# Performance work log

Measured on AMD Instinct MI355X. Metric: run time of the kernel, lower is better.

## Reference

```python
import jax, jax.numpy as jnp
import numpy as np

B, S, D = 4, 2048, 1024
H = 16
HD = D // H


def setup_inputs() -> dict:
    key = jax.random.key(0)
    ks = jax.random.split(key, 6)
    s = 1.0 / np.sqrt(D)
    x = jax.random.normal(ks[0], (B, S, D), dtype=jnp.float32)
    Wq = jax.random.uniform(ks[1], (D, D), jnp.float32, -s, s)
    Wk = jax.random.uniform(ks[2], (D, D), jnp.float32, -s, s)
    Wv = jax.random.uniform(ks[3], (D, D), jnp.float32, -s, s)
    Wo = jax.random.uniform(ks[4], (D, D), jnp.float32, -s, s)
    bo = jax.random.uniform(ks[5], (D,), jnp.float32, -s, s)
    return {"x": x, "Wq": Wq, "Wk": Wk, "Wv": Wv, "Wo": Wo, "bo": bo}


def reference(x, Wq, Wk, Wv, Wo, bo):
    b, n, _ = x.shape
    # QKV projections (nn.Linear applies x @ W.T; W here stored as [d_in, d_out])
    q = (x @ Wq).reshape(b, n, H, HD).transpose(0, 2, 1, 3)  # [b,h,s,hd]
    k = (x @ Wk).reshape(b, n, H, HD).transpose(0, 2, 1, 3)
    v = (x @ Wv).reshape(b, n, H, HD).transpose(0, 2, 1, 3)
    scores = jnp.einsum('bhqd,bhkd->bhqk', q, k) / np.sqrt(HD).astype(np.float32)
    causal = jnp.tril(jnp.ones((n, n), dtype=bool))  # True = keep
    scores = jnp.where(causal, scores, -jnp.inf)
    attn = jax.nn.softmax(scores, axis=-1)
    ctx = jnp.einsum('bhqk,bhkd->bhqd', attn, v)  # [b,h,s,hd]
    ctx = ctx.transpose(0, 2, 1, 3).reshape(b, n, D)
    return ctx @ Wo + bo
```

## Files before the change

kernel.cpp:

```cpp
#include <hip/hip_runtime.h>

#define NB 4
#define NS 2048
#define ND 1024
#define NH 16
#define NHD 64
#define NTOK (NB*NS)

typedef float f32x4 __attribute__((ext_vector_type(4)));
typedef __bf16 bf16x8 __attribute__((ext_vector_type(8)));
typedef __bf16 bf16x4 __attribute__((ext_vector_type(4)));

#define MFMA16(a,b,c) __builtin_amdgcn_mfma_f32_16x16x32_bf16((a),(b),(c),0,0,0)
#define SBAR() __builtin_amdgcn_s_barrier()
#define VMCNT(n) asm volatile("s_waitcnt vmcnt(" #n ")" ::: "memory")
#define LGKM(n) asm volatile("s_waitcnt lgkmcnt(" #n ")" ::: "memory")
#define SCHEDB() __builtin_amdgcn_sched_barrier(0)

__device__ __forceinline__ float fexp2(float x) {
#if __has_builtin(__builtin_amdgcn_exp2f)
  return __builtin_amdgcn_exp2f(x);
#else
  return __expf(x * 0.69314718056f);
#endif
}

__device__ __forceinline__ void gload_lds16(const __bf16* g, const __bf16* l) {
  __builtin_amdgcn_global_load_lds(
      (const __attribute__((address_space(1))) void*)(uintptr_t)(const void*)g,
      (__attribute__((address_space(3))) void*)(uint32_t)(uintptr_t)(const void*)l,
      16, 0, 0);
}

__global__ void k_convert_x(const float* __restrict__ x, __bf16* __restrict__ xb) {
  int i = blockIdx.x * blockDim.x + threadIdx.x;
  float4 v = ((const float4*)x)[i];
  bf16x4 o = { (__bf16)v.x, (__bf16)v.y, (__bf16)v.z, (__bf16)v.w };
  ((bf16x4*)xb)[i] = o;
}

__global__ void k_transpose_w(const float* __restrict__ w0, const float* __restrict__ w1,
                              const float* __restrict__ w2, const float* __restrict__ w3,
                              __bf16* __restrict__ wqkvt, __bf16* __restrict__ wot) {
  __shared__ float tl[64][65];
  const int z = blockIdx.z;
  const float* src = (z==0)?w0:(z==1)?w1:(z==2)?w2:w3;
  __bf16* dst = (z<3) ? (wqkvt + (size_t)z*ND*ND) : wot;
  const int kb = blockIdx.x*64, nb = blockIdx.y*64;
  const int c = threadIdx.x & 63, r0 = threadIdx.x >> 6;
  for (int i=0;i<16;i++) { int r = r0*16+i; tl[r][c] = src[(size_t)(kb+r)*ND + nb + c]; }
  __syncthreads();
  for (int i=0;i<16;i++) { int r = r0*16+i; dst[(size_t)(nb+r)*ND + kb + c] = (__bf16)tl[c][r]; }
}

__global__ __launch_bounds__(512, 4) void k_gemm_qkv(
    const __bf16* __restrict__ A, const __bf16* __restrict__ Bt,
    __bf16* __restrict__ qs, __bf16* __restrict__ ks, __bf16* __restrict__ vt) {
  constexpr int BUFE = (256+128)*32;
  __shared__ __align__(16) __bf16 lds[3*BUFE];
  const int tid = threadIdx.x;
  const int wid = tid>>6, lane = tid&63;
  const int wr = wid>>1, wc = wid&1;
  const int lrow = lane&15, lg = lane>>4;
  const int srow4 = lane>>2;
  const int scol  = ((lane&3) ^ ((lane>>3)&3))*8;

  const int id  = blockIdx.x;
  const int xcd = id & 7;
  const int nl  = id >> 3;
  const int st  = nl >> 5;
  const int u   = nl & 31;
  const int bx  = xcd*4 + (u >> 3);
  const int by  = st*8 + (u & 7);
  const int m0 = bx*256, n0 = by*128;

  auto stage = [&](int t, int bsel) {
    __bf16* buf = lds + bsel*BUFE;
    const int k0 = t*32;
    #pragma unroll
    for (int i=0;i<2;i++) {
      int c = wid + i*8;
      gload_lds16(A + (size_t)(m0 + c*16 + srow4)*ND + k0 + scol, buf + c*512);
    }
    gload_lds16(Bt + (size_t)(n0 + wid*16 + srow4)*ND + k0 + scol, buf + 8192 + wid*512);
  };

  const int slot = (lg ^ ((lrow>>1)&3)) << 4;
  const int abase = (wr*64 + lrow)*64 + slot;
  const int bbase = 16384 + (wc*64 + lrow)*64 + slot;

  f32x4 acc[4][4];
  f32x4 zero = {0.f,0.f,0.f,0.f};
  #pragma unroll
  for (int i=0;i<4;i++) for (int j=0;j<4;j++) acc[i][j] = zero;

  stage(0,0);
  stage(1,1);
  for (int t=0; t<32; ++t) {
    if (t < 30) stage(t+2, (t+2)%3);
    if (t < 30)      { VMCNT(6); }
    else if (t == 30){ VMCNT(3); }
    else             { VMCNT(0); }
    SBAR();
    const char* L = (const char*)(lds + (t%3)*BUFE);
    bf16x8 bfr[4], af[4];
    #pragma unroll
    for (int cb=0;cb<4;cb++) bfr[cb] = *(const bf16x8*)(L + bbase + cb*1024);
    #pragma unroll
    for (int mf=0;mf<2;mf++) af[mf] = *(const bf16x8*)(L + abase + mf*1024);
    SCHEDB();
    #pragma unroll
    for (int mf=2;mf<4;mf++) af[mf] = *(const bf16x8*)(L + abase + mf*1024);
    LGKM(2);
    SCHEDB();
    __builtin_amdgcn_s_setprio(1);
    #pragma unroll
    for (int mf=0;mf<2;mf++)
      #pragma unroll
      for (int cb=0;cb<4;cb++)
        acc[mf][cb] = MFMA16(af[mf], bfr[cb], acc[mf][cb]);
    __builtin_amdgcn_s_setprio(0);
    LGKM(0);
    SCHEDB();
    __builtin_amdgcn_s_setprio(1);
    #pragma unroll
    for (int mf=2;mf<4;mf++)
      #pragma unroll
      for (int cb=0;cb<4;cb++)
        acc[mf][cb] = MFMA16(af[mf], bfr[cb], acc[mf][cb]);
    __builtin_amdgcn_s_setprio(0);
    SBAR();
  }

  const int which = by >> 3;
  const int h = (by&7)*2 + wc;
  __bf16* ws = lds + wid*4096;
  const int tokbase = m0 + wr*64;
  const int b = tokbase >> 11, s0 = tokbase & 2047;

  if (which < 2) {
    __bf16* dst = which ? ks : qs;
    #pragma unroll
    for (int mf=0;mf<4;mf++)
      #pragma unroll
      for (int cb=0;cb<4;cb++)
        #pragma unroll
        for (int r=0;r<4;r++) {
          int row = mf*16 + lg*4 + r;
          int chunk = (cb*2 + (lrow>>3)) ^ (row&7);
          *(__bf16*)((char*)ws + row*128 + chunk*16 + (lrow&7)*2) = (__bf16)acc[mf][cb][r];
        }
    #pragma unroll
    for (int p=0;p<8;p++) {
      int row = p*8 + (lane>>3);
      int chunk = (lane&7) ^ (row&7);
      bf16x8 v = *(const bf16x8*)((char*)ws + row*128 + chunk*16);
      *(bf16x8*)(dst + ((size_t)(b*NH + h)*NS + s0 + row)*NHD + (lane&7)*8) = v;
    }
  } else {
    #pragma unroll
    for (int mf=0;mf<4;mf++)
      #pragma unroll
      for (int cb=0;cb<4;cb++) {
        bf16x4 pk = { (__bf16)acc[mf][cb][0], (__bf16)acc[mf][cb][1],
                      (__bf16)acc[mf][cb][2], (__bf16)acc[mf][cb][3] };
        int ldsrow = cb*16 + lrow;
        int chunk = (mf*2 + (lg>>1)) ^ (ldsrow&7);
        *(bf16x4*)((char*)ws + ldsrow*128 + chunk*16 + (lg&1)*8) = pk;
      }
    #pragma unroll
    for (int p=0;p<8;p++) {
      int hd = p*8 + (lane>>3);
      int chunk = (lane&7) ^ (hd&7);
      bf16x8 v = *(const bf16x8*)((char*)ws + hd*128 + chunk*16);
      *(bf16x8*)(vt + ((size_t)(b*NH + h)*NHD + hd)*NS + s0 + (lane&7)*8) = v;
    }
  }
}

__global__ __launch_bounds__(512, 2) void k_gemm_out(
    const __bf16* __restrict__ A, const __bf16* __restrict__ Bt,
    const float* __restrict__ bo, float* __restrict__ out) {
  constexpr int BUFE = (256+128)*64;
  __shared__ __align__(16) __bf16 lds[3*BUFE];
  const int tid = threadIdx.x;
  const int wid = tid>>6, lane = tid&63;
  const int wr = wid>>1, wc = wid&1;
  const int lrow = lane&15, lg = lane>>4;
  const int srow = lane>>3;
  const int scol = ((lane&7) ^ srow)*8;

  const int id  = blockIdx.x;
  const int xcd = id & 7;
  const int nl  = id >> 3;
  const int bx  = xcd*4 + (nl >> 3);
  const int by  = nl & 7;
  const int m0 = bx*256, n0 = by*128;

  auto stage = [&](int t, int bsel) {
    __bf16* buf = lds + bsel*BUFE;
    const int k0 = t*64;
    #pragma unroll
    for (int i=0;i<4;i++) {
      int c = wid + i*8;
      gload_lds16(A + (size_t)(m0 + c*8 + srow)*ND + k0 + scol, buf + c*512);
    }
    #pragma unroll
    for (int i=0;i<2;i++) {
      int c = wid + i*8;
      gload_lds16(Bt + (size_t)(n0 + c*8 + srow)*ND + k0 + scol, buf + 16384 + c*512);
    }
  };

  int kx[8];
  #pragma unroll
  for (int kk=0;kk<8;kk++) kx[kk] = ((kk ^ (lrow&7)) << 4);
  const int abase = (wr*64 + lrow)*128;
  const int bbase = 32768 + (wc*64 + lrow)*128;

  f32x4 acc[4][4];
  f32x4 zero = {0.f,0.f,0.f,0.f};
  #pragma unroll
  for (int i=0;i<4;i++) for (int j=0;j<4;j++) acc[i][j] = zero;

  stage(0,0);
  stage(1,1);
  for (int t=0; t<16; ++t) {
    if (t < 14) stage(t+2, (t+2)%3);
    if (t < 14)      { VMCNT(12); }
    else if (t == 14){ VMCNT(6);  }
    else             { VMCNT(0);  }
    SBAR();
    const char* L = (const char*)(lds + (t%3)*BUFE);
    bf16x8 bfr[4][2], af[4][2];
    #pragma unroll
    for (int cb=0;cb<4;cb++)
      #pragma unroll
      for (int ksi=0;ksi<2;ksi++)
        bfr[cb][ksi] = *(const bf16x8*)(L + bbase + cb*2048 + kx[ksi*4+lg]);
    #pragma unroll
    for (int mf=0;mf<2;mf++)
      #pragma unroll
      for (int ksi=0;ksi<2;ksi++)
        af[mf][ksi] = *(const bf16x8*)(L + abase + mf*2048 + kx[ksi*4+lg]);
    SCHEDB();
    #pragma unroll
    for (int mf=2;mf<4;mf++)
      #pragma unroll
      for (int ksi=0;ksi<2;ksi++)
        af[mf][ksi] = *(const bf16x8*)(L + abase + mf*2048 + kx[ksi*4+lg]);
    LGKM(4);
    SCHEDB();
    __builtin_amdgcn_s_setprio(1);
    #pragma unroll
    for (int mf=0;mf<2;mf++)
      #pragma unroll
      for (int cb=0;cb<4;cb++)
        #pragma unroll
        for (int ksi=0;ksi<2;ksi++)
          acc[mf][cb] = MFMA16(af[mf][ksi], bfr[cb][ksi], acc[mf][cb]);
    __builtin_amdgcn_s_setprio(0);
    LGKM(0);
    SCHEDB();
    __builtin_amdgcn_s_setprio(1);
    #pragma unroll
    for (int mf=2;mf<4;mf++)
      #pragma unroll
      for (int cb=0;cb<4;cb++)
        #pragma unroll
        for (int ksi=0;ksi<2;ksi++)
          acc[mf][cb] = MFMA16(af[mf][ksi], bfr[cb][ksi], acc[mf][cb]);
    __builtin_amdgcn_s_setprio(0);
    SBAR();
  }

  #pragma unroll
  for (int cb=0;cb<4;cb++) {
    const int n = n0 + wc*64 + cb*16 + lrow;
    const float bias = bo[n];
    #pragma unroll
    for (int mf=0;mf<4;mf++)
      #pragma unroll
      for (int r=0;r<4;r++) {
        const int m = m0 + wr*64 + mf*16 + lg*4 + r;
        out[(size_t)m*ND + n] = acc[mf][cb][r] + bias;
      }
  }
}

__global__ __launch_bounds__(256, 3) void k_attn(
    const __bf16* __restrict__ qs, const __bf16* __restrict__ ks,
    const __bf16* __restrict__ vt, __bf16* __restrict__ ctx) {
  __shared__ __align__(16) __bf16 sK[2][64*64];
  __shared__ __align__(16) __bf16 sV[2][64*64];
  __shared__ __align__(16) __bf16 sP[4][32*72];
  const int tid = threadIdx.x, w = tid >> 6, lane = tid & 63;
  const int lrow = lane & 15, lg = lane >> 4;
  const int bh = blockIdx.x;
  const int bq = 15 - blockIdx.y;
  const int nt = 2*bq + 2;
  const size_t base = (size_t)bh * NS * NHD;
  const __bf16* Kg = ks + base;
  const __bf16* Vg = vt + base;
  __bf16* sPw = sP[w];

  const int q0w = bq*128 + w*32;
  bf16x8 qf[2][2];
  for (int rb=0;rb<2;rb++)
    for (int kk=0;kk<2;kk++) {
      bf16x8 v = *(const bf16x8*)(qs + base + (size_t)(q0w + rb*16 + lrow)*NHD + kk*32 + lg*8);
      bf16x8 o;
      for (int j=0;j<8;j++) o[j] = (__bf16)((float)v[j] * 0.1803368801f);
      qf[rb][kk] = o;
    }

  int koffB[4][2];
  for (int cb=0;cb<4;cb++) {
    int r = cb*16 + lrow;
    for (int kk=0;kk<2;kk++)
      koffB[cb][kk] = r*128 + (((kk*4 + lg) ^ (r & 7)) << 4);
  }
  const int s_r[2]  = { (w + 0)*8 + (lane>>3), (w + 4)*8 + (lane>>3) };
  const int s_u[2]  = { (lane&7) ^ (s_r[0]&7), (lane&7) ^ (s_r[1]&7) };

  f32x4 zero = {0.f,0.f,0.f,0.f};
  f32x4 oacc[2][4];
  float psum[2] = {0.f, 0.f};
  for (int rb=0;rb<2;rb++) for(int cb=0;cb<4;cb++) oacc[rb][cb]=zero;

  for (int i=0;i<2;i++) {
    gload_lds16(Kg + (size_t)s_r[i]*NHD + s_u[i]*8,              sK[0] + (w + i*4)*512);
    gload_lds16(Vg + (size_t)s_r[i]*NS  + s_u[i]*8,              sV[0] + (w + i*4)*512);
  }
  asm volatile("s_waitcnt vmcnt(0)" ::: "memory");
  __syncthreads();

  int buf = 0;
  for (int t = 0; t < nt; ++t) {
    if (t+1 < nt) {
      const __bf16* Kt = Kg + (size_t)(t+1)*64*NHD;
      for (int i=0;i<2;i++) {
        gload_lds16(Kt + (size_t)s_r[i]*NHD + s_u[i]*8,          sK[buf^1] + (w + i*4)*512);
        gload_lds16(Vg + (size_t)s_r[i]*NS + (t+1)*64 + s_u[i]*8, sV[buf^1] + (w + i*4)*512);
      }
    }
    if (!(t == nt-1 && w < 2)) {
      const __bf16* bK = sK[buf];
      const __bf16* bV = sV[buf];
      const bool bdry = (t >= nt-2);
      for (int cb=0;cb<4;cb++) {
        bf16x8 kf0 = *(const bf16x8*)((const char*)bK + koffB[cb][0]);
        bf16x8 kf1 = *(const bf16x8*)((const char*)bK + koffB[cb][1]);
        const int kvb = t*64 + cb*16 + lg*4;
        for (int rb=0;rb<2;rb++) {
          f32x4 s4 = MFMA16(kf0, qf[rb][0], zero);
          s4 = MFMA16(kf1, qf[rb][1], s4);
          const int qg = q0w + rb*16 + lrow;
          float e0 = fexp2(s4[0]), e1 = fexp2(s4[1]);
          float e2 = fexp2(s4[2]), e3 = fexp2(s4[3]);
          if (bdry) {
            if (kvb + 0 > qg) e0 = 0.f;
            if (kvb + 1 > qg) e1 = 0.f;
            if (kvb + 2 > qg) e2 = 0.f;
            if (kvb + 3 > qg) e3 = 0.f;
          }
          psum[rb] += (e0 + e1) + (e2 + e3);
          bf16x4 pk = { (__bf16)e0, (__bf16)e1, (__bf16)e2, (__bf16)e3 };
          *(bf16x4*)(sPw + (rb*16 + lrow)*72 + cb*16 + lg*4) = pk;
        }
      }
      for (int kk=0;kk<2;kk++) {
        bf16x8 pa0 = *(const bf16x8*)(sPw + (lrow)*72      + kk*32 + lg*8);
        bf16x8 pa1 = *(const bf16x8*)(sPw + (16 + lrow)*72 + kk*32 + lg*8);
        for (int cb=0;cb<4;cb++) {
          bf16x8 vb = *(const bf16x8*)((const char*)bV + koffB[cb][kk]);
          oacc[0][cb] = MFMA16(pa0, vb, oacc[0][cb]);
          oacc[1][cb] = MFMA16(pa1, vb, oacc[1][cb]);
        }
      }
    }
    asm volatile("s_waitcnt vmcnt(0)" ::: "memory");
    __syncthreads();
    buf ^= 1;
  }

  float inv[2];
  for (int rb=0;rb<2;rb++) {
    float s = psum[rb];
    s += __shfl_xor(s, 16);
    s += __shfl_xor(s, 32);
    inv[rb] = 1.0f / s;
  }

  __bf16* ws = &sK[0][0] + w*2048;
  const int b = bh >> 4, h = bh & 15;
  for (int rb=0;rb<2;rb++)
    for (int cb=0;cb<4;cb++)
      for (int r=0;r<4;r++) {
        int row = rb*16 + lg*4 + r;
        float nrm = __shfl(inv[rb], lg*4 + r);
        int chunk = (cb*2 + (lrow>>3)) ^ (row&7);
        *(__bf16*)((char*)ws + row*128 + chunk*16 + (lrow&7)*2) =
            (__bf16)(oacc[rb][cb][r] * nrm);
      }
  for (int p=0;p<4;p++) {
    int row = p*8 + (lane>>3);
    int chunk = (lane&7) ^ (row&7);
    bf16x8 v = *(const bf16x8*)((char*)ws + row*128 + chunk*16);
    int q = q0w + row;
    *(bf16x8*)(ctx + ((size_t)(b*NS + q))*ND + h*NHD + (lane&7)*8) = v;
  }
}

extern "C" void kernel_launch(void* const* d_in, const int* in_sizes, int n_in,
                              void* d_out, int out_size, void* d_ws, size_t ws_size,
                              hipStream_t stream) {
  const float* x  = (const float*)d_in[0];
  const float* Wq = (const float*)d_in[1];
  const float* Wk = (const float*)d_in[2];
  const float* Wv = (const float*)d_in[3];
  const float* Wo = (const float*)d_in[4];
  const float* bo = (const float*)d_in[5];
  float* out = (float*)d_out;

  __bf16* xb    = (__bf16*)d_ws;
  __bf16* wqkvt = xb    + (size_t)NTOK*ND;
  __bf16* wot   = wqkvt + (size_t)3*ND*ND;
  __bf16* qsc   = wot   + (size_t)ND*ND;
  __bf16* ksc   = qsc   + (size_t)NTOK*ND;
  __bf16* vtc   = ksc   + (size_t)NTOK*ND;
  __bf16* ctx   = vtc   + (size_t)NTOK*ND;

  k_convert_x<<<NTOK*ND/(4*256), 256, 0, stream>>>(x, xb);
  k_transpose_w<<<dim3(ND/64, ND/64, 4), 256, 0, stream>>>(Wq, Wk, Wv, Wo, wqkvt, wot);
  k_gemm_qkv<<<768, 512, 0, stream>>>(xb, wqkvt, qsc, ksc, vtc);
  k_attn<<<dim3(NB*NH, NS/128), 256, 0, stream>>>(qsc, ksc, vtc, ctx);
  k_gemm_out<<<256, 512, 0, stream>>>(ctx, wot, bo, out);
}
```

Measured before the change: 145.1 us.

## Double QKV GEMM K-tile and interleave prefetch with MFMA quarters; merge prep kernels

The QKV GEMM now stages 64-wide K tiles instead of 32, which halves the number of main-loop iterations. It uses a new 8-way XOR swizzle and splits each iteration into four MFMA quarters, with the next tile's global-to-LDS loads issued between them. This is meant to cut barrier and loop overhead and to hide load latency behind compute. LDS use doubles, so occupancy drops and launch_bounds is lowered to 2 blocks per unit. The x conversion and weight transpose kernels are also merged into a single launch to save one kernel launch.

```diff
diff --git a/kernel.cpp b/kernel.cpp
--- a/kernel.cpp
+++ b/kernel.cpp
@@ -32,38 +32,41 @@
       16, 0, 0);
 }
 
-__global__ void k_convert_x(const float* __restrict__ x, __bf16* __restrict__ xb) {
-  int i = blockIdx.x * blockDim.x + threadIdx.x;
-  float4 v = ((const float4*)x)[i];
-  bf16x4 o = { (__bf16)v.x, (__bf16)v.y, (__bf16)v.z, (__bf16)v.w };
-  ((bf16x4*)xb)[i] = o;
-}
-
-__global__ void k_transpose_w(const float* __restrict__ w0, const float* __restrict__ w1,
-                              const float* __restrict__ w2, const float* __restrict__ w3,
-                              __bf16* __restrict__ wqkvt, __bf16* __restrict__ wot) {
+__global__ void k_prep(const float* __restrict__ x,
+                       const float* __restrict__ w0, const float* __restrict__ w1,
+                       const float* __restrict__ w2, const float* __restrict__ w3,
+                       __bf16* __restrict__ xb, __bf16* __restrict__ wqkvt,
+                       __bf16* __restrict__ wot) {
   __shared__ float tl[64][65];
-  const int z = blockIdx.z;
-  const float* src = (z==0)?w0:(z==1)?w1:(z==2)?w2:w3;
-  __bf16* dst = (z<3) ? (wqkvt + (size_t)z*ND*ND) : wot;
-  const int kb = blockIdx.x*64, nb = blockIdx.y*64;
-  const int c = threadIdx.x & 63, r0 = threadIdx.x >> 6;
-  for (int i=0;i<16;i++) { int r = r0*16+i; tl[r][c] = src[(size_t)(kb+r)*ND + nb + c]; }
-  __syncthreads();
-  for (int i=0;i<16;i++) { int r = r0*16+i; dst[(size_t)(nb+r)*ND + kb + c] = (__bf16)tl[c][r]; }
-}
-
-__global__ __launch_bounds__(512, 4) void k_gemm_qkv(
+  const int bi = blockIdx.x;
+  if (bi < 1024) {
+    const int z = bi >> 8, rem = bi & 255;
+    const float* src = (z==0)?w0:(z==1)?w1:(z==2)?w2:w3;
+    __bf16* dst = (z<3) ? (wqkvt + (size_t)z*ND*ND) : wot;
+    const int kb = (rem>>4)*64, nb = (rem&15)*64;
+    const int c = threadIdx.x & 63, r0 = threadIdx.x >> 6;
+    for (int i=0;i<16;i++) { int r = r0*16+i; tl[r][c] = src[(size_t)(kb+r)*ND + nb + c]; }
+    __syncthreads();
+    for (int i=0;i<16;i++) { int r = r0*16+i; dst[(size_t)(nb+r)*ND + kb + c] = (__bf16)tl[c][r]; }
+  } else {
+    const int i = (bi - 1024)*256 + threadIdx.x;
+    float4 v = ((const float4*)x)[i];
+    bf16x4 o = { (__bf16)v.x, (__bf16)v.y, (__bf16)v.z, (__bf16)v.w };
+    ((bf16x4*)xb)[i] = o;
+  }
+}
+
+__global__ __launch_bounds__(512, 2) void k_gemm_qkv(
     const __bf16* __restrict__ A, const __bf16* __restrict__ Bt,
     __bf16* __restrict__ qs, __bf16* __restrict__ ks, __bf16* __restrict__ vt) {
-  constexpr int BUFE = (256+128)*32;
+  constexpr int BUFE = (256+128)*64;
   __shared__ __align__(16) __bf16 lds[3*BUFE];
   const int tid = threadIdx.x;
   const int wid = tid>>6, lane = tid&63;
   const int wr = wid>>1, wc = wid&1;
   const int lrow = lane&15, lg = lane>>4;
-  const int srow4 = lane>>2;
-  const int scol  = ((lane&3) ^ ((lane>>3)&3))*8;
+  const int srow = lane>>3;
+  const int scol = ((lane&7) ^ srow)*8;
 
   const int id  = blockIdx.x;
   const int xcd = id & 7;
@@ -74,60 +77,113 @@
   const int by  = st*8 + (u & 7);
   const int m0 = bx*256, n0 = by*128;
 
-  auto stage = [&](int t, int bsel) {
-    __bf16* buf = lds + bsel*BUFE;
-    const int k0 = t*32;
-    #pragma unroll
-    for (int i=0;i<2;i++) {
-      int c = wid + i*8;
-      gload_lds16(A + (size_t)(m0 + c*16 + srow4)*ND + k0 + scol, buf + c*512);
-    }
-    gload_lds16(Bt + (size_t)(n0 + wid*16 + srow4)*ND + k0 + scol, buf + 8192 + wid*512);
+  auto stageA = [&](int t, int bsel, int i) {
+    int c = wid + i*8;
+    gload_lds16(A + (size_t)(m0 + c*8 + srow)*ND + t*64 + scol,
+                lds + bsel*BUFE + c*512);
   };
-
-  const int slot = (lg ^ ((lrow>>1)&3)) << 4;
-  const int abase = (wr*64 + lrow)*64 + slot;
-  const int bbase = 16384 + (wc*64 + lrow)*64 + slot;
+  auto stageB = [&](int t, int bsel, int i) {
+    int c = wid + i*8;
+    gload_lds16(Bt + (size_t)(n0 + c*8 + srow)*ND + t*64 + scol,
+                lds + bsel*BUFE + 16384 + c*512);
+  };
+
+  int kx[8];
+  #pragma unroll
+  for (int kk=0;kk<8;kk++) kx[kk] = ((kk ^ (lrow&7)) << 4);
+  const int abase = (wr*64 + lrow)*128;
+  const int bbase = 32768 + (wc*64 + lrow)*128;
 
   f32x4 acc[4][4];
   f32x4 zero = {0.f,0.f,0.f,0.f};
   #pragma unroll
   for (int i=0;i<4;i++) for (int j=0;j<4;j++) acc[i][j] = zero;
 
-  stage(0,0);
-  stage(1,1);
-  for (int t=0; t<32; ++t) {
-    if (t < 30) stage(t+2, (t+2)%3);
-    if (t < 30)      { VMCNT(6); }
-    else if (t == 30){ VMCNT(3); }
-    else             { VMCNT(0); }
+  #pragma unroll
+  for (int i=0;i<4;i++) stageA(0,0,i);
+  #pragma unroll
+  for (int i=0;i<2;i++) stageB(0,0,i);
+  #pragma unroll
+  for (int i=0;i<4;i++) stageA(1,1,i);
+  #pragma unroll
+  for (int i=0;i<2;i++) stageB(1,1,i);
+
+  for (int t=0; t<16; ++t) {
+    if (t < 15) { VMCNT(6); } else { VMCNT(0); }
     SBAR();
     const char* L = (const char*)(lds + (t%3)*BUFE);
-    bf16x8 bfr[4], af[4];
-    #pragma unroll
-    for (int cb=0;cb<4;cb++) bfr[cb] = *(const bf16x8*)(L + bbase + cb*1024);
-    #pragma unroll
-    for (int mf=0;mf<2;mf++) af[mf] = *(const bf16x8*)(L + abase + mf*1024);
-    SCHEDB();
-    #pragma unroll
-    for (int mf=2;mf<4;mf++) af[mf] = *(const bf16x8*)(L + abase + mf*1024);
-    LGKM(2);
-    SCHEDB();
-    __builtin_amdgcn_s_setprio(1);
+    const int tn = t+2, bs = (t+2)%3;
+    const bool pf = (tn < 16);
+    bf16x8 af[4][2], bfr[4][2];
+
     #pragma unroll
     for (int mf=0;mf<2;mf++)
       #pragma unroll
-      for (int cb=0;cb<4;cb++)
-        acc[mf][cb] = MFMA16(af[mf], bfr[cb], acc[mf][cb]);
-    __builtin_amdgcn_s_setprio(0);
-    LGKM(0);
-    SCHEDB();
-    __builtin_amdgcn_s_setprio(1);
+      for (int ksi=0;ksi<2;ksi++)
+        af[mf][ksi] = *(const bf16x8*)(L + abase + mf*2048 + kx[ksi*4+lg]);
+    #pragma unroll
+    for (int cb=0;cb<2;cb++)
+      #pragma unroll
+      for (int ksi=0;ksi<2;ksi++)
+        bfr[cb][ksi] = *(const bf16x8*)(L + bbase + cb*2048 + kx[ksi*4+lg]);
+    if (pf) { stageA(tn,bs,0); stageA(tn,bs,1); }
+    SBAR(); LGKM(0); SCHEDB();
+    __builtin_amdgcn_s_setprio(1);
+    #pragma unroll
+    for (int mf=0;mf<2;mf++)
+      #pragma unroll
+      for (int cb=0;cb<2;cb++)
+        #pragma unroll
+        for (int ksi=0;ksi<2;ksi++)
+          acc[mf][cb] = MFMA16(af[mf][ksi], bfr[cb][ksi], acc[mf][cb]);
+    __builtin_amdgcn_s_setprio(0);
+    SBAR();
+
+    #pragma unroll
+    for (int cb=2;cb<4;cb++)
+      #pragma unroll
+      for (int ksi=0;ksi<2;ksi++)
+        bfr[cb][ksi] = *(const bf16x8*)(L + bbase + cb*2048 + kx[ksi*4+lg]);
+    if (pf) { stageA(tn,bs,2); stageA(tn,bs,3); }
+    SBAR(); LGKM(0); SCHEDB();
+    __builtin_amdgcn_s_setprio(1);
+    #pragma unroll
+    for (int mf=0;mf<2;mf++)
+      #pragma unroll
+      for (int cb=2;cb<4;cb++)
+        #pragma unroll
+        for (int ksi=0;ksi<2;ksi++)
+          acc[mf][cb] = MFMA16(af[mf][ksi], bfr[cb][ksi], acc[mf][cb]);
+    __builtin_amdgcn_s_setprio(0);
+    SBAR();
+
     #pragma unroll
     for (int mf=2;mf<4;mf++)
       #pragma unroll
-      for (int cb=0;cb<4;cb++)
-        acc[mf][cb] = MFMA16(af[mf], bfr[cb], acc[mf][cb]);
+      for (int ksi=0;ksi<2;ksi++)
+        af[mf][ksi] = *(const bf16x8*)(L + abase + mf*2048 + kx[ksi*4+lg]);
+    if (pf) { stageB(tn,bs,0); stageB(tn,bs,1); }
+    SBAR(); LGKM(0); SCHEDB();
+    __builtin_amdgcn_s_setprio(1);
+    #pragma unroll
+    for (int mf=2;mf<4;mf++)
+      #pragma unroll
+      for (int cb=0;cb<2;cb++)
+        #pragma unroll
+        for (int ksi=0;ksi<2;ksi++)
+          acc[mf][cb] = MFMA16(af[mf][ksi], bfr[cb][ksi], acc[mf][cb]);
+    __builtin_amdgcn_s_setprio(0);
+    SBAR();
+
+    SBAR(); SCHEDB();
+    __builtin_amdgcn_s_setprio(1);
+    #pragma unroll
+    for (int mf=2;mf<4;mf++)
+      #pragma unroll
+      for (int cb=2;cb<4;cb++)
+        #pragma unroll
+        for (int ksi=0;ksi<2;ksi++)
+          acc[mf][cb] = MFMA16(af[mf][ksi], bfr[cb][ksi], acc[mf][cb]);
     __builtin_amdgcn_s_setprio(0);
     SBAR();
   }
@@ -431,8 +487,7 @@
   __bf16* vtc   = ksc   + (size_t)NTOK*ND;
   __bf16* ctx   = vtc   + (size_t)NTOK*ND;
 
-  k_convert_x<<<NTOK*ND/(4*256), 256, 0, stream>>>(x, xb);
-  k_transpose_w<<<dim3(ND/64, ND/64, 4), 256, 0, stream>>>(Wq, Wk, Wv, Wo, wqkvt, wot);
+  k_prep<<<1024 + NTOK*ND/(4*256), 256, 0, stream>>>(x, Wq, Wk, Wv, Wo, xb, wqkvt, wot);
   k_gemm_qkv<<<768, 512, 0, stream>>>(xb, wqkvt, qsc, ksc, vtc);
   k_attn<<<dim3(NB*NH, NS/128), 256, 0, stream>>>(qsc, ksc, vtc, ctx);
   k_gemm_out<<<256, 512, 0, stream>>>(ctx, wot, bo, out);
```

New measurement: 144.8 us. No clear change (-0.2%).
